# Optimization experiments

Measured on AMD Instinct MI355X. Metric: run time of the kernel, lower is better.

The kernel has to match this reference:

```python
import jax, jax.numpy as jnp
import numpy as np

B, S, H, E, V, EXTRA = 128, 512, 1024, 1024, 50000, 500
EPS = 1e-8


def setup_inputs() -> dict:
    key = jax.random.key(0)
    ks = jax.random.split(key, 32)
    sc = 0.02
    n = lambda k, sh: (jax.random.normal(k, sh, jnp.float32) * sc)
    return {
        'inputs': jax.random.randint(ks[0], (B, 1), 0, V),
        'dec_hidden': n(ks[1], (1, B, H)),
        'enc_outputs': n(ks[2], (B, S, H)),
        'enc_padding_mask': jnp.zeros((B, S), jnp.float32),
        'context_vector_t1': n(ks[3], (B, H)),
        'enc_batch_extend_vocab': jax.random.randint(ks[4], (B, S), 0, V + EXTRA),
        'extra_zeros': jnp.zeros((B, EXTRA), jnp.float32),
        'coverage': jax.random.uniform(ks[5], (B, S), jnp.float32) * 0.1,
        # parameters
        'embed': n(ks[6], (V, E)),
        'ln_g': jnp.ones((E,), jnp.float32),
        'ln_b': jnp.zeros((E,), jnp.float32),
        'xc_W': n(ks[7], (E, H + E)), 'xc_b': jnp.zeros((E,), jnp.float32),
        'W_ih': n(ks[8], (3 * H, E)), 'W_hh': n(ks[9], (3 * H, H)),
        'b_ih': jnp.zeros((3 * H,), jnp.float32), 'b_hh': jnp.zeros((3 * H,), jnp.float32),
        'Wh': n(ks[10], (H, H)),
        'Ws': n(ks[11], (H, H)), 'Ws_b': jnp.zeros((H,), jnp.float32),
        'Wc': n(ks[12], (H, 1)),
        'Vv': n(ks[13], (H,)),
        'pg_W': n(ks[14], (2 * H + E,)), 'pg_b': jnp.zeros((1,), jnp.float32),
        'out1_W': n(ks[15], (H, 2 * H)), 'out1_b': jnp.zeros((H,), jnp.float32),
        'out2_W': n(ks[16], (V, H)), 'out2_b': jnp.zeros((V,), jnp.float32),
    }


def _layernorm(x, g, b):
    mu = jnp.mean(x, axis=-1, keepdims=True)
    var = jnp.mean(jnp.square(x - mu), axis=-1, keepdims=True)
    return (x - mu) / jnp.sqrt(var + 1e-5) * g + b


def reference(inputs, dec_hidden, enc_outputs, enc_padding_mask, context_vector_t1,
              enc_batch_extend_vocab, extra_zeros, coverage,
              embed, ln_g, ln_b, xc_W, xc_b, W_ih, W_hh, b_ih, b_hh,
              Wh, Ws, Ws_b, Wc, Vv, pg_W, pg_b, out1_W, out1_b, out2_W, out2_b):
    # embedding + layernorm: [B, E]
    x = _layernorm(embed[inputs[:, 0]], ln_g, ln_b)
    # x_context: Linear(H+E -> E)
    x = jnp.concatenate([x, context_vector_t1], axis=1) @ xc_W.T + xc_b

    # single GRU step (torch gate order r, z, n)
    h0 = dec_hidden[0]  # [B, H]
    gx = x @ W_ih.T + b_ih
    gh = h0 @ W_hh.T + b_hh
    r = jax.nn.sigmoid(gx[:, :H] + gh[:, :H])
    z = jax.nn.sigmoid(gx[:, H:2 * H] + gh[:, H:2 * H])
    nn_ = jnp.tanh(gx[:, 2 * H:] + r * gh[:, 2 * H:])
    s_t = (1.0 - z) * nn_ + z * h0  # [B, H]; dec_output == s_t for 1-layer GRU
    dec_output = s_t

    # Bahdanau additive attention with coverage
    enc_feat = jnp.einsum('bsh,kh->bsk', enc_outputs, Wh)           # [B,S,H]
    dec_feat = s_t @ Ws.T + Ws_b                                     # [B,H]
    cov_feat = coverage[:, :, None] * Wc[:, 0][None, None, :]        # [B,S,H]
    e_t = jnp.einsum('bsh,h->bs', jnp.tanh(enc_feat + dec_feat[:, None, :] + cov_feat), Vv)
    atten_dist = jax.nn.softmax(e_t + enc_padding_mask, axis=1)      # [B,S]
    h_t = jnp.einsum('bs,bsh->bh', atten_dist, enc_outputs)          # [B,H]
    coverage_next = coverage + atten_dist

    # pointer generator gate
    p_gen_in = jnp.concatenate([h_t, s_t, x], axis=1)                # [B, 2H+E]
    p_gen = jnp.clip(jax.nn.sigmoid(p_gen_in @ pg_W + pg_b), EPS, None)[:, None]  # [B,1]

    # vocab distribution
    s_t_h_t = jnp.concatenate([dec_output, h_t], axis=1)             # [B,2H]
    logits = (s_t_h_t @ out1_W.T + out1_b) @ out2_W.T + out2_b       # [B,V]
    vocab_dist = jax.nn.softmax(logits, axis=1)

    # mix + scatter-add copy distribution over extended vocab
    vocab_dist_ = jnp.concatenate([p_gen * vocab_dist, extra_zeros], axis=1)  # [B, V+EXTRA]
    atten_dist_ = (1.0 - p_gen) * atten_dist
    rows = jnp.arange(B)[:, None]
    final_dist = vocab_dist_.at[rows, enc_batch_extend_vocab].add(atten_dist_)
    final_dist = jnp.clip(final_dist, EPS, None)

    coverage_loss = jnp.sum(jnp.minimum(atten_dist, coverage_next), axis=1)  # [B]
    return (jnp.log(final_dist), s_t[None], h_t, coverage_next, coverage_loss)
```

## Files before the change

### kernel.cpp

```cpp
#include <hip/hip_runtime.h>
#include <hip/hip_bf16.h>
#include <stdint.h>

#define B_ 128
#define S_ 512
#define H_ 1024
#define E_ 1024
#define V_ 50000
#define EXTRA_ 500
#define VE_ 50500
#define EPS_ 1e-8f

typedef __attribute__((ext_vector_type(4))) float f32x4;
typedef __attribute__((ext_vector_type(8))) short bf16x8;

__device__ __forceinline__ unsigned short f2bf(float f) {
    unsigned u = __builtin_bit_cast(unsigned, f);
    u = (u + 0x7FFFu + ((u >> 16) & 1u)) >> 16;
    return (unsigned short)u;
}

__device__ __forceinline__ bf16x8 pack8(const float* f) {
    union { bf16x8 v; unsigned short s[8]; } u;
#pragma unroll
    for (int i = 0; i < 8; ++i) u.s[i] = f2bf(f[i]);
    return u.v;
}

__device__ __forceinline__ float bf2f(unsigned short s) {
    unsigned u = (unsigned)s << 16;
    return __builtin_bit_cast(float, u);
}

__device__ __forceinline__ float fast_tanh(float x) {
    x = fminf(fmaxf(x, -15.f), 15.f);
    float e = __expf(2.f * x);
    return __fdividef(e - 1.f, e + 1.f);
}

__device__ __forceinline__ void gload16(const void* g, void* l) {
    __builtin_amdgcn_global_load_lds(
        reinterpret_cast<const __attribute__((address_space(1))) unsigned int*>(
            reinterpret_cast<uintptr_t>(g)),
        reinterpret_cast<__attribute__((address_space(3))) unsigned int*>(
            reinterpret_cast<uintptr_t>(l)),
        16, 0, 0);
}

__global__ __launch_bounds__(256) void prep_kernel(
    const float* __restrict__ enc, const float* __restrict__ wh,
    unsigned short* __restrict__ enc_bf, unsigned short* __restrict__ wh_bf,
    const int* __restrict__ tok, const float* __restrict__ embed,
    const float* __restrict__ g, const float* __restrict__ beta,
    const float* __restrict__ ctx, float* __restrict__ x_cat)
{
    __shared__ float red[256];
    int bid = blockIdx.x, t = threadIdx.x;
    if (bid < 33280) {
        const float* in; unsigned short* out; int i;
        if (bid < 512) { in = wh;  out = wh_bf;  i = (bid * 256 + t) * 8; }
        else           { in = enc; out = enc_bf; i = ((bid - 512) * 256 + t) * 8; }
        float f[8];
        *(float4*)f     = *(const float4*)(in + i);
        *(float4*)(f+4) = *(const float4*)(in + i + 4);
        union { uint4 v; unsigned short s[8]; } u;
#pragma unroll
        for (int j = 0; j < 8; ++j) u.s[j] = f2bf(f[j]);
        *(uint4*)(out + i) = u.v;
        return;
    }
    int b = bid - 33280;
    const float* row = embed + (size_t)tok[b] * E_;
    float v[4];
    float s = 0.f;
#pragma unroll
    for (int i = 0; i < 4; ++i) { v[i] = row[t + i*256]; s += v[i]; }
    red[t] = s; __syncthreads();
    for (int o = 128; o > 0; o >>= 1) { if (t < o) red[t] += red[t+o]; __syncthreads(); }
    float mu = red[0] * (1.f/E_);
    __syncthreads();
    s = 0.f;
#pragma unroll
    for (int i = 0; i < 4; ++i) { float d = v[i]-mu; s += d*d; }
    red[t] = s; __syncthreads();
    for (int o = 128; o > 0; o >>= 1) { if (t < o) red[t] += red[t+o]; __syncthreads(); }
    float inv = rsqrtf(red[0]*(1.f/E_) + 1e-5f);
    float* xrow = x_cat + (size_t)b * 2048;
#pragma unroll
    for (int i = 0; i < 4; ++i) {
        int j = t + i*256;
        xrow[j] = (v[i]-mu)*inv*g[j] + beta[j];
        xrow[1024 + j] = ctx[b*1024 + j];
    }
}

__global__ __launch_bounds__(256) void embed_ln_kernel(
    const int* __restrict__ tok, const float* __restrict__ embed,
    const float* __restrict__ g, const float* __restrict__ beta,
    const float* __restrict__ ctx, float* __restrict__ x_cat)
{
    __shared__ float red[256];
    int b = blockIdx.x, t = threadIdx.x;
    const float* row = embed + (size_t)tok[b] * E_;
    float v[4];
    float s = 0.f;
#pragma unroll
    for (int i = 0; i < 4; ++i) { v[i] = row[t + i*256]; s += v[i]; }
    red[t] = s; __syncthreads();
    for (int o = 128; o > 0; o >>= 1) { if (t < o) red[t] += red[t+o]; __syncthreads(); }
    float mu = red[0] * (1.f/E_);
    __syncthreads();
    s = 0.f;
#pragma unroll
    for (int i = 0; i < 4; ++i) { float d = v[i]-mu; s += d*d; }
    red[t] = s; __syncthreads();
    for (int o = 128; o > 0; o >>= 1) { if (t < o) red[t] += red[t+o]; __syncthreads(); }
    float inv = rsqrtf(red[0]*(1.f/E_) + 1e-5f);
    float* xrow = x_cat + (size_t)b * 2048;
#pragma unroll
    for (int i = 0; i < 4; ++i) {
        int j = t + i*256;
        xrow[j] = (v[i]-mu)*inv*g[j] + beta[j];
        xrow[1024 + j] = ctx[b*1024 + j];
    }
}

__global__ __launch_bounds__(256) void gemm128_kernel(
    const float* __restrict__ A, const float* __restrict__ W,
    const float* __restrict__ bias, float* __restrict__ C,
    int N, int K, int ldc, int kchunk)
{
    __shared__ char Ab[128*64*2];
    __shared__ char Wb[64*64*2];
    const int t = threadIdx.x;
    const int wid = t >> 6, lane = t & 63;
    const int waveM = wid >> 1, waveN = wid & 1;
    const int lq = lane >> 4, lr = lane & 15;
    const int n0 = blockIdx.x * 64;
    const int kbeg = blockIdx.y * kchunk, kend = kbeg + kchunk;
    f32x4 acc[4][2];
#pragma unroll
    for (int i = 0; i < 4; ++i)
#pragma unroll
        for (int j = 0; j < 2; ++j) acc[i][j] = (f32x4){0.f,0.f,0.f,0.f};
    for (int kc = kbeg; kc < kend; kc += 64) {
        __syncthreads();
#pragma unroll
        for (int i = 0; i < 4; ++i) {
            int c = t + i*256;
            int row = c >> 3, k8 = (c & 7) << 3;
            const float* src = A + (size_t)row*K + kc + k8;
            float f[8];
            *(float4*)f     = *(const float4*)src;
            *(float4*)(f+4) = *(const float4*)(src+4);
            int byte = row*128 + ((k8*2) ^ ((row&7)<<4));
            *(bf16x8*)(Ab + byte) = pack8(f);
        }
#pragma unroll
        for (int i = 0; i < 2; ++i) {
            int c = t + i*256;
            int row = c >> 3, k8 = (c & 7) << 3;
            int n = n0 + row;
            float f[8] = {0,0,0,0,0,0,0,0};
            if (n < N) {
                const float* src = W + (size_t)n*K + kc + k8;
                *(float4*)f     = *(const float4*)src;
                *(float4*)(f+4) = *(const float4*)(src+4);
            }
            int byte = row*128 + ((k8*2) ^ ((row&7)<<4));
            *(bf16x8*)(Wb + byte) = pack8(f);
        }
        __syncthreads();
#pragma unroll
        for (int kf = 0; kf < 2; ++kf) {
            int kk2 = (kf*32 + (lq<<3)) * 2;
            bf16x8 bfr[2];
#pragma unroll
            for (int nf = 0; nf < 2; ++nf) {
                int r = waveN*32 + nf*16 + lr;
                bfr[nf] = *(const bf16x8*)(Wb + r*128 + (kk2 ^ ((r&7)<<4)));
            }
#pragma unroll
            for (int mf = 0; mf < 4; ++mf) {
                int r = waveM*64 + mf*16 + lr;
                bf16x8 afr = *(const bf16x8*)(Ab + r*128 + (kk2 ^ ((r&7)<<4)));
#pragma unroll
                for (int nf = 0; nf < 2; ++nf)
                    acc[mf][nf] = __builtin_amdgcn_mfma_f32_16x16x32_bf16(afr, bfr[nf], acc[mf][nf], 0, 0, 0);
            }
        }
    }
    float* Cp = C + (size_t)blockIdx.y * 128 * (size_t)ldc;
    bool addb = (bias != nullptr) && (blockIdx.y == 0);
#pragma unroll
    for (int mf = 0; mf < 4; ++mf)
#pragma unroll
        for (int nf = 0; nf < 2; ++nf) {
            int n = n0 + waveN*32 + nf*16 + lr;
            if (n < N) {
                float bv = addb ? bias[n] : 0.f;
#pragma unroll
                for (int r = 0; r < 4; ++r) {
                    int m = waveM*64 + mf*16 + (lq<<2) + r;
                    Cp[(size_t)m*ldc + n] = acc[mf][nf][r] + bv;
                }
            }
        }
}

__global__ __launch_bounds__(256) void gemm128_dual_kernel(
    const float* __restrict__ A0, const float* __restrict__ W0,
    const float* __restrict__ b0, float* __restrict__ C0, int ap0,
    const float* __restrict__ A1, const float* __restrict__ W1,
    const float* __restrict__ b1, float* __restrict__ C1, int ap1,
    int N, int K, int ldc, int kchunk)
{
    __shared__ char Ab[128*64*2];
    __shared__ char Wb[64*64*2];
    const float* A = blockIdx.z ? A1 : A0;
    const float* W = blockIdx.z ? W1 : W0;
    const float* bias = blockIdx.z ? b1 : b0;
    float* C = blockIdx.z ? C1 : C0;
    const int ap = blockIdx.z ? ap1 : ap0;
    const int t = threadIdx.x;
    const int wid = t >> 6, lane = t & 63;
    const int waveM = wid >> 1, waveN = wid & 1;
    const int lq = lane >> 4, lr = lane & 15;
    const int n0 = blockIdx.x * 64;
    const int kbeg = blockIdx.y * kchunk, kend = kbeg + kchunk;
    f32x4 acc[4][2];
#pragma unroll
    for (int i = 0; i < 4; ++i)
#pragma unroll
        for (int j = 0; j < 2; ++j) acc[i][j] = (f32x4){0.f,0.f,0.f,0.f};
    for (int kc = kbeg; kc < kend; kc += 64) {
        __syncthreads();
#pragma unroll
        for (int i = 0; i < 4; ++i) {
            int c = t + i*256;
            int row = c >> 3, k8 = (c & 7) << 3;
            const float* src = A + (size_t)row*K + kc + k8;
            float f[8];
            *(float4*)f     = *(const float4*)src;
            *(float4*)(f+4) = *(const float4*)(src+4);
            if (ap == 4) {
#pragma unroll
                for (int p = 1; p < 4; ++p) {
                    float g0[8];
                    *(float4*)g0     = *(const float4*)(src + p*131072);
                    *(float4*)(g0+4) = *(const float4*)(src + p*131072 + 4);
#pragma unroll
                    for (int j = 0; j < 8; ++j) f[j] += g0[j];
                }
            }
            int byte = row*128 + ((k8*2) ^ ((row&7)<<4));
            *(bf16x8*)(Ab + byte) = pack8(f);
        }
#pragma unroll
        for (int i = 0; i < 2; ++i) {
            int c = t + i*256;
            int row = c >> 3, k8 = (c & 7) << 3;
            int n = n0 + row;
            float f[8] = {0,0,0,0,0,0,0,0};
            if (n < N) {
                const float* src = W + (size_t)n*K + kc + k8;
                *(float4*)f     = *(const float4*)src;
                *(float4*)(f+4) = *(const float4*)(src+4);
            }
            int byte = row*128 + ((k8*2) ^ ((row&7)<<4));
            *(bf16x8*)(Wb + byte) = pack8(f);
        }
        __syncthreads();
#pragma unroll
        for (int kf = 0; kf < 2; ++kf) {
            int kk2 = (kf*32 + (lq<<3)) * 2;
            bf16x8 bfr[2];
#pragma unroll
            for (int nf = 0; nf < 2; ++nf) {
                int r = waveN*32 + nf*16 + lr;
                bfr[nf] = *(const bf16x8*)(Wb + r*128 + (kk2 ^ ((r&7)<<4)));
            }
#pragma unroll
            for (int mf = 0; mf < 4; ++mf) {
                int r = waveM*64 + mf*16 + lr;
                bf16x8 afr = *(const bf16x8*)(Ab + r*128 + (kk2 ^ ((r&7)<<4)));
#pragma unroll
                for (int nf = 0; nf < 2; ++nf)
                    acc[mf][nf] = __builtin_amdgcn_mfma_f32_16x16x32_bf16(afr, bfr[nf], acc[mf][nf], 0, 0, 0);
            }
        }
    }
    float* Cp = C + (size_t)blockIdx.y * 128 * (size_t)ldc;
    bool addb = (bias != nullptr) && (blockIdx.y == 0);
#pragma unroll
    for (int mf = 0; mf < 4; ++mf)
#pragma unroll
        for (int nf = 0; nf < 2; ++nf) {
            int n = n0 + waveN*32 + nf*16 + lr;
            if (n < N) {
                float bv = addb ? bias[n] : 0.f;
#pragma unroll
                for (int r = 0; r < 4; ++r) {
                    int m = waveM*64 + mf*16 + (lq<<2) + r;
                    Cp[(size_t)m*ldc + n] = acc[mf][nf][r] + bv;
                }
            }
        }
}

__global__ __launch_bounds__(256) void reduce4_kernel(
    const float* __restrict__ in, float* __restrict__ out, int len)
{
    int i = blockIdx.x*256 + threadIdx.x;
    if (i < len) out[i] = in[i] + in[len+i] + in[2*len+i] + in[3*len+i];
}

__global__ __launch_bounds__(256) void gru_gate_kernel(
    const float* __restrict__ gxp, const float* __restrict__ ghp,
    const float* __restrict__ h0, float* __restrict__ s_t)
{
    int i = blockIdx.x*256 + threadIdx.x;
    int b = i >> 10, h = i & 1023;
    const float* gx0 = gxp + (size_t)b*3072;
    const float* gx1 = gx0 + 393216;
    const float* gh0 = ghp + (size_t)b*3072;
    const float* gh1 = gh0 + 393216;
    float grx = gx0[h] + gx1[h],        grh = gh0[h] + gh1[h];
    float gzx = gx0[h+1024]+gx1[h+1024], gzh = gh0[h+1024]+gh1[h+1024];
    float gnx = gx0[h+2048]+gx1[h+2048], gnh = gh0[h+2048]+gh1[h+2048];
    float r = 1.f/(1.f+__expf(-(grx + grh)));
    float z = 1.f/(1.f+__expf(-(gzx + gzh)));
    float n = fast_tanh(gnx + r*gnh);
    s_t[i] = (1.f-z)*n + z*h0[i];
}

__global__ __launch_bounds__(256,4) void attn_gemm_bf16_kernel(
    const unsigned short* __restrict__ encb,
    const unsigned short* __restrict__ whb,
    const float* __restrict__ ds_part,
    const float* __restrict__ coverage,
    const float* __restrict__ Wc, const float* __restrict__ Vv,
    float* __restrict__ e_part)
{
    __shared__ char Ab[128*128];
    __shared__ char Bb[128*128];
    const int t = threadIdx.x;
    const int wid = t >> 6, lane = t & 63;
    const int waveM = wid >> 1, waveN = wid & 1;
    const int lq = lane >> 4, lr = lane & 15;
    int bid = blockIdx.x;
    int wg = (bid & 7) * 512 + (bid >> 3);
    const int nt = wg & 7, mt = wg >> 3;
    const int m0 = mt * 128, n0 = nt * 128;
    const int b = m0 >> 9;

    const int grow = wid*8 + (lane >> 3);
    const int gk16 = (lane & 7) ^ ((lane >> 3) & 7);
    const unsigned short* asrc = encb + (size_t)(m0 + grow)*H_ + gk16*8;
    const unsigned short* bsrc = whb  + (size_t)(n0 + grow)*H_ + gk16*8;
    char* aldst = Ab + wid*1024;
    char* bldst = Bb + wid*1024;

    f32x4 acc[4][4];
#pragma unroll
    for (int i = 0; i < 4; ++i)
#pragma unroll
        for (int j = 0; j < 4; ++j) acc[i][j] = (f32x4){0.f,0.f,0.f,0.f};

    for (int kc = 0; kc < 1024; kc += 64) {
        __syncthreads();
#pragma unroll
        for (int i = 0; i < 4; ++i) {
            gload16(asrc + kc + i*32*H_, aldst + i*4096);
            gload16(bsrc + kc + i*32*H_, bldst + i*4096);
        }
        __syncthreads();
#pragma unroll
        for (int kf = 0; kf < 2; ++kf) {
            const int koff = kf*64 + lq*16;
            bf16x8 bfr[4];
#pragma unroll
            for (int nf = 0; nf < 4; ++nf) {
                int r = waveN*64 + nf*16 + lr;
                bfr[nf] = *(const bf16x8*)(Bb + r*128 + (koff ^ ((r&7)<<4)));
            }
#pragma unroll
            for (int mf = 0; mf < 4; ++mf) {
                int r = waveM*64 + mf*16 + lr;
                bf16x8 afr = *(const bf16x8*)(Ab + r*128 + (koff ^ ((r&7)<<4)));
#pragma unroll
                for (int nf = 0; nf < 4; ++nf)
                    acc[mf][nf] = __builtin_amdgcn_mfma_f32_16x16x32_bf16(afr, bfr[nf], acc[mf][nf], 0, 0, 0);
            }
        }
    }
    float cv[4][4];
#pragma unroll
    for (int mf = 0; mf < 4; ++mf)
#pragma unroll
        for (int r = 0; r < 4; ++r) {
            int m = m0 + waveM*64 + mf*16 + lq*4 + r;
            cv[mf][r] = coverage[b*S_ + (m & 511)];
        }
    float e_acc[4][4] = {};
#pragma unroll
    for (int nf = 0; nf < 4; ++nf) {
        int n = n0 + waveN*64 + nf*16 + lr;
        const float* dsp = ds_part + b*H_ + n;
        float df = dsp[0] + dsp[131072] + dsp[262144] + dsp[393216];
        float wc = Wc[n];
        float vv = Vv[n];
#pragma unroll
        for (int mf = 0; mf < 4; ++mf)
#pragma unroll
            for (int r = 0; r < 4; ++r)
                e_acc[mf][r] += fast_tanh(acc[mf][nf][r] + df + cv[mf][r]*wc) * vv;
    }
#pragma unroll
    for (int msk = 1; msk < 16; msk <<= 1)
#pragma unroll
        for (int mf = 0; mf < 4; ++mf)
#pragma unroll
            for (int r = 0; r < 4; ++r)
                e_acc[mf][r] += __shfl_xor(e_acc[mf][r], msk);
    __syncthreads();
    float* el = (float*)Ab;
    if (lr == 0) {
#pragma unroll
        for (int mf = 0; mf < 4; ++mf)
#pragma unroll
            for (int r = 0; r < 4; ++r)
                el[waveN*128 + waveM*64 + mf*16 + lq*4 + r] = e_acc[mf][r];
    }
    __syncthreads();
    if (t < 128)
        e_part[(size_t)nt*65536 + m0 + t] = el[t] + el[128 + t];
}

__global__ __launch_bounds__(512,4) void attn_gemm_f32_kernel(
    const float* __restrict__ enc, const float* __restrict__ Wh,
    const float* __restrict__ ds_part, const float* __restrict__ coverage,
    const float* __restrict__ Wc, const float* __restrict__ Vv,
    float* __restrict__ e_part)
{
    __shared__ char Ab[128*64*2];
    __shared__ char Bb[256*64*2];
    __shared__ float e_lds[4][128];
    const int t = threadIdx.x;
    const int wid = t >> 6, lane = t & 63;
    const int waveM = wid >> 2, waveN = wid & 3;
    const int lq = lane >> 4, lr = lane & 15;
    int bid = blockIdx.x;
    int wg = (bid & 7) * 256 + (bid >> 3);
    const int mt = wg >> 2, nt = wg & 3;
    const int m0 = mt * 128, n0 = nt * 256;
    const int b = m0 >> 9;
    const int arow = t >> 2, ak0 = (t & 3) * 16;
    const int brow = t >> 1, bk0 = (t & 1) * 32;
    f32x4 acc[4][4];
#pragma unroll
    for (int i = 0; i < 4; ++i)
#pragma unroll
        for (int j = 0; j < 4; ++j) acc[i][j] = (f32x4){0.f,0.f,0.f,0.f};
    for (int kc = 0; kc < 1024; kc += 64) {
        __syncthreads();
        {
            const float* src = enc + (size_t)(m0 + arow)*H_ + kc + ak0;
            float f[16];
            *(float4*)(f)    = *(const float4*)(src);
            *(float4*)(f+4)  = *(const float4*)(src+4);
            *(float4*)(f+8)  = *(const float4*)(src+8);
            *(float4*)(f+12) = *(const float4*)(src+12);
            char* dst = Ab + arow*128;
            int sw = (arow & 7) << 4;
            *(bf16x8*)(dst + ((ak0*2)      ^ sw)) = pack8(f);
            *(bf16x8*)(dst + ((ak0*2 + 16) ^ sw)) = pack8(f+8);
        }
        {
            const float* src = Wh + (size_t)(n0 + brow)*H_ + kc + bk0;
            char* dst = Bb + brow*128;
            int sw = (brow & 7) << 4;
            float f[16];
            *(float4*)(f)    = *(const float4*)(src);
            *(float4*)(f+4)  = *(const float4*)(src+4);
            *(float4*)(f+8)  = *(const float4*)(src+8);
            *(float4*)(f+12) = *(const float4*)(src+12);
            *(bf16x8*)(dst + ((bk0*2)      ^ sw)) = pack8(f);
            *(bf16x8*)(dst + ((bk0*2 + 16) ^ sw)) = pack8(f+8);
            *(float4*)(f)    = *(const float4*)(src+16);
            *(float4*)(f+4)  = *(const float4*)(src+20);
            *(float4*)(f+8)  = *(const float4*)(src+24);
            *(float4*)(f+12) = *(const float4*)(src+28);
            *(bf16x8*)(dst + ((bk0*2 + 32) ^ sw)) = pack8(f);
            *(bf16x8*)(dst + ((bk0*2 + 48) ^ sw)) = pack8(f+8);
        }
        __syncthreads();
#pragma unroll
        for (int kf = 0; kf < 2; ++kf) {
            const int koff = kf*64 + lq*16;
            bf16x8 bfr[4];
#pragma unroll
            for (int nf = 0; nf < 4; ++nf) {
                int r = waveN*64 + nf*16 + lr;
                bfr[nf] = *(const bf16x8*)(Bb + r*128 + (koff ^ ((r&7)<<4)));
            }
#pragma unroll
            for (int mf = 0; mf < 4; ++mf) {
                int r = waveM*64 + mf*16 + lr;
                bf16x8 afr = *(const bf16x8*)(Ab + r*128 + (koff ^ ((r&7)<<4)));
#pragma unroll
                for (int nf = 0; nf < 4; ++nf)
                    acc[mf][nf] = __builtin_amdgcn_mfma_f32_16x16x32_bf16(afr, bfr[nf], acc[mf][nf], 0, 0, 0);
            }
        }
    }
    float cv[4][4];
#pragma unroll
    for (int mf = 0; mf < 4; ++mf)
#pragma unroll
        for (int r = 0; r < 4; ++r) {
            int m = m0 + waveM*64 + mf*16 + lq*4 + r;
            cv[mf][r] = coverage[b*S_ + (m & 511)];
        }
    float e_acc[4][4] = {};
#pragma unroll
    for (int nf = 0; nf < 4; ++nf) {
        int n = n0 + waveN*64 + nf*16 + lr;
        const float* dsp = ds_part + b*H_ + n;
        float df = dsp[0] + dsp[131072] + dsp[262144] + dsp[393216];
        float wc = Wc[n];
        float vv = Vv[n];
#pragma unroll
        for (int mf = 0; mf < 4; ++mf)
#pragma unroll
            for (int r = 0; r < 4; ++r)
                e_acc[mf][r] += fast_tanh(acc[mf][nf][r] + df + cv[mf][r]*wc) * vv;
    }
#pragma unroll
    for (int msk = 1; msk < 16; msk <<= 1)
#pragma unroll
        for (int mf = 0; mf < 4; ++mf)
#pragma unroll
            for (int r = 0; r < 4; ++r)
                e_acc[mf][r] += __shfl_xor(e_acc[mf][r], msk);
    if (lr == 0) {
#pragma unroll
        for (int mf = 0; mf < 4; ++mf)
#pragma unroll
            for (int r = 0; r < 4; ++r)
                e_lds[waveN][waveM*64 + mf*16 + lq*4 + r] = e_acc[mf][r];
    }
    __syncthreads();
    if (t < 128)
        e_part[(size_t)nt*65536 + m0 + t] = e_lds[0][t] + e_lds[1][t] + e_lds[2][t] + e_lds[3][t];
}

__global__ __launch_bounds__(256) void attn_softmax_kernel(
    const float* __restrict__ e_part, int np, const float* __restrict__ mask,
    const float* __restrict__ cov, float* __restrict__ att,
    float* __restrict__ cov_next, float* __restrict__ loss)
{
    __shared__ float red[256];
    int b = blockIdx.x, t = threadIdx.x;
    int i1 = b*S_ + t, i2 = i1 + 256;
    float e1 = mask[i1], e2 = mask[i2];
    for (int p = 0; p < np; ++p) { e1 += e_part[(size_t)p*65536 + i1]; e2 += e_part[(size_t)p*65536 + i2]; }
    red[t] = fmaxf(e1, e2); __syncthreads();
    for (int o = 128; o > 0; o >>= 1) { if (t < o) red[t] = fmaxf(red[t], red[t+o]); __syncthreads(); }
    float m = red[0]; __syncthreads();
    float a1 = __expf(e1-m), a2 = __expf(e2-m);
    red[t] = a1+a2; __syncthreads();
    for (int o = 128; o > 0; o >>= 1) { if (t < o) red[t] += red[t+o]; __syncthreads(); }
    float inv = 1.f/red[0]; __syncthreads();
    a1 *= inv; a2 *= inv;
    att[i1] = a1; att[i2] = a2;
    float c1 = cov[i1]+a1, c2 = cov[i2]+a2;
    cov_next[i1] = c1; cov_next[i2] = c2;
    red[t] = fminf(a1,c1)+fminf(a2,c2); __syncthreads();
    for (int o = 128; o > 0; o >>= 1) { if (t < o) red[t] += red[t+o]; __syncthreads(); }
    if (t == 0) loss[b] = red[0];
}

__global__ __launch_bounds__(256) void smax_ctx_bf16_kernel(
    const float* __restrict__ e_part, const float* __restrict__ mask,
    const float* __restrict__ cov, const unsigned short* __restrict__ encb,
    float* __restrict__ att, float* __restrict__ cov_next, float* __restrict__ loss,
    float* __restrict__ hq)
{
    __shared__ float red[256];
    __shared__ float asl[512];
    __shared__ float cpart[128][9];
    int b = blockIdx.x, q = blockIdx.y, t = threadIdx.x;
    int i1 = b*S_ + t, i2 = i1 + 256;
    float e1 = mask[i1], e2 = mask[i2];
#pragma unroll
    for (int p = 0; p < 8; ++p) { e1 += e_part[(size_t)p*65536 + i1]; e2 += e_part[(size_t)p*65536 + i2]; }
    red[t] = fmaxf(e1, e2); __syncthreads();
    for (int o = 128; o > 0; o >>= 1) { if (t < o) red[t] = fmaxf(red[t], red[t+o]); __syncthreads(); }
    float m = red[0]; __syncthreads();
    float a1 = __expf(e1-m), a2 = __expf(e2-m);
    red[t] = a1+a2; __syncthreads();
    for (int o = 128; o > 0; o >>= 1) { if (t < o) red[t] += red[t+o]; __syncthreads(); }
    float inv = 1.f/red[0]; __syncthreads();
    a1 *= inv; a2 *= inv;
    asl[t] = a1; asl[t+256] = a2;
    if (q == 0) {
        att[i1] = a1; att[i2] = a2;
        float c1 = cov[i1]+a1, c2 = cov[i2]+a2;
        cov_next[i1] = c1; cov_next[i2] = c2;
        red[t] = fminf(a1,c1)+fminf(a2,c2); __syncthreads();
        for (int o = 128; o > 0; o >>= 1) { if (t < o) red[t] += red[t+o]; __syncthreads(); }
        if (t == 0) loss[b] = red[0];
    }
    __syncthreads();
    int lane = t & 127, su = t >> 7;
    int hc = lane * 8;
    const unsigned short* ep = encb + ((size_t)(b*S_ + q*128 + su*64))*H_ + hc;
    const float* aw = asl + q*128 + su*64;
    float acc[8] = {};
#pragma unroll 2
    for (int s = 0; s < 64; ++s) {
        uint4 v = *(const uint4*)(ep + (size_t)s*H_);
        float w = aw[s];
        const unsigned short* pv = (const unsigned short*)&v;
#pragma unroll
        for (int k = 0; k < 8; ++k) acc[k] += w * bf2f(pv[k]);
    }
    if (su == 1) {
#pragma unroll
        for (int k = 0; k < 8; ++k) cpart[lane][k] = acc[k];
    }
    __syncthreads();
    if (su == 0) {
        float o[8];
#pragma unroll
        for (int k = 0; k < 8; ++k) o[k] = acc[k] + cpart[lane][k];
        float* dst = hq + (size_t)q*131072 + (size_t)b*1024 + hc;
        *(float4*)dst     = *(float4*)o;
        *(float4*)(dst+4) = *(float4*)(o+4);
    }
}

__global__ __launch_bounds__(256) void context_part_f32_kernel(
    const float* __restrict__ att, const float* __restrict__ enc, float* __restrict__ hq)
{
    __shared__ float asl[128];
    int b = blockIdx.x, sub = blockIdx.y;
    int hh = sub & 1, q = sub >> 1;
    int t = threadIdx.x;
    if (t < 128) asl[t] = att[b*S_ + q*128 + t];
    __syncthreads();
    int h = hh*512 + t*2;
    const float* ep = enc + (size_t)b*S_*H_ + (size_t)q*128*H_ + h;
    float a0 = 0.f, a1 = 0.f;
#pragma unroll 4
    for (int s = 0; s < 128; ++s) {
        float2 v = *(const float2*)(ep + (size_t)s*H_);
        float w = asl[s];
        a0 += w*v.x; a1 += w*v.y;
    }
    float* o = hq + ((size_t)q*B_ + b)*H_ + h;
    o[0] = a0; o[1] = a1;
}

__global__ __launch_bounds__(256) void pgen_kernel(
    const float* __restrict__ hq, const float* __restrict__ s_t, const float* __restrict__ x_part,
    const float* __restrict__ pgW, const float* __restrict__ pgb,
    float* __restrict__ pgen, float* __restrict__ h_t, float* __restrict__ A2)
{
    __shared__ float red[256];
    int b = blockIdx.x, t = threadIdx.x;
    float dot = 0.f;
#pragma unroll
    for (int i = 0; i < 4; ++i) {
        int j = t + i*256;
        const float* hp = hq + (size_t)b*1024 + j;
        float hv = hp[0] + hp[131072] + hp[262144] + hp[393216];
        const float* xp = x_part + (size_t)b*1024 + j;
        float xv = xp[0] + xp[131072] + xp[262144] + xp[393216];
        float sv = s_t[b*1024 + j];
        h_t[b*1024 + j] = hv;
        A2[(size_t)b*2048 + j] = sv;
        A2[(size_t)b*2048 + 1024 + j] = hv;
        dot += hv*pgW[j] + sv*pgW[1024+j] + xv*pgW[2048+j];
    }
    red[t] = dot; __syncthreads();
    for (int o = 128; o > 0; o >>= 1) { if (t < o) red[t] += red[t+o]; __syncthreads(); }
    if (t == 0) {
        float p = 1.f/(1.f+__expf(-(red[0] + pgb[0])));
        pgen[b] = fmaxf(p, EPS_);
    }
}

__global__ __launch_bounds__(256) void vocab_pass1_kernel(
    const float* __restrict__ logits, float2* __restrict__ mpart)
{
    __shared__ float rm[256], rl[256];
    int b = blockIdx.x, c = blockIdx.y, t = threadIdx.x;
    int lo = c * 12625;
    int hi = min(lo + 12625, V_);
    const float* row = logits + (size_t)b*VE_;
    float m = -1e30f, l = 0.f;
    for (int i = lo + t; i < hi; i += 256) {
        float v = row[i];
        if (v > m) { l = l*__expf(m-v) + 1.f; m = v; }
        else l += __expf(v-m);
    }
    rm[t] = m; rl[t] = l; __syncthreads();
    for (int o = 128; o > 0; o >>= 1) {
        if (t < o) {
            float m1 = rm[t], m2 = rm[t+o];
            float M = fmaxf(m1, m2);
            rl[t] = rl[t]*__expf(m1-M) + rl[t+o]*__expf(m2-M);
            rm[t] = M;
        }
        __syncthreads();
    }
    if (t == 0) mpart[b*4 + c] = make_float2(rm[0], rl[0]);
}

__global__ __launch_bounds__(256) void vocab_pass2_kernel(
    const float* __restrict__ logits, const float2* __restrict__ mpart,
    const float* __restrict__ pgen, const int* __restrict__ ebev,
    const float* __restrict__ att, float* __restrict__ out0)
{
    __shared__ unsigned bmap[395];
    __shared__ unsigned hkey[1024];
    __shared__ float hval[1024];
    int b = blockIdx.x, c = blockIdx.y, t = threadIdx.x;
    int lo = c * 12625, hi = lo + 12625;
    float2 q0 = mpart[b*4+0], q1 = mpart[b*4+1], q2 = mpart[b*4+2], q3 = mpart[b*4+3];
    float M = fmaxf(fmaxf(q0.x, q1.x), fmaxf(q2.x, q3.x));
    float L = q0.y*__expf(q0.x-M) + q1.y*__expf(q1.x-M) + q2.y*__expf(q2.x-M) + q3.y*__expf(q3.x-M);
    float pg = pgen[b];
    float inv = pg / L;
    for (int i = t; i < 395; i += 256) bmap[i] = 0u;
    for (int i = t; i < 1024; i += 256) { hkey[i] = 0xFFFFFFFFu; hval[i] = 0.f; }
    __syncthreads();
    for (int s = t; s < 512; s += 256) {
        int col = ebev[b*S_ + s];
        if (col >= lo && col < hi) {
            float v = (1.f - pg) * att[b*S_ + s];
            unsigned cl = (unsigned)(col - lo);
            atomicOr(&bmap[cl >> 5], 1u << (cl & 31));
            unsigned slot = (cl * 2654435761u >> 16) & 1023u;
            while (true) {
                unsigned old = atomicCAS(&hkey[slot], 0xFFFFFFFFu, cl);
                if (old == 0xFFFFFFFFu || old == cl) { atomicAdd(&hval[slot], v); break; }
                slot = (slot + 1) & 1023u;
            }
        }
    }
    __syncthreads();
    const float* row = logits + (size_t)b*VE_;
    float* orow = out0 + (size_t)b*VE_;
    for (int i = lo + t; i < hi; i += 256) {
        float base = 0.f;
        if (i < V_) base = __expf(row[i] - M) * inv;
        unsigned cl = (unsigned)(i - lo);
        if (bmap[cl >> 5] & (1u << (cl & 31))) {
            unsigned slot = (cl * 2654435761u >> 16) & 1023u;
            while (hkey[slot] != cl) slot = (slot + 1) & 1023u;
            base += hval[slot];
        }
        orow[i] = __logf(fmaxf(base, EPS_));
    }
}

extern "C" void kernel_launch(void* const* d_in, const int* in_sizes, int n_in,
                              void* d_out, int out_size, void* d_ws, size_t ws_size,
                              hipStream_t stream) {
    const int*   tok        = (const int*)d_in[0];
    const float* dec_hidden = (const float*)d_in[1];
    const float* enc        = (const float*)d_in[2];
    const float* mask       = (const float*)d_in[3];
    const float* ctx1       = (const float*)d_in[4];
    const int*   ebev       = (const int*)d_in[5];
    const float* cov        = (const float*)d_in[7];
    const float* embed      = (const float*)d_in[8];
    const float* ln_g       = (const float*)d_in[9];
    const float* ln_b       = (const float*)d_in[10];
    const float* xc_W       = (const float*)d_in[11];
    const float* xc_b       = (const float*)d_in[12];
    const float* W_ih       = (const float*)d_in[13];
    const float* W_hh       = (const float*)d_in[14];
    const float* b_ih       = (const float*)d_in[15];
    const float* b_hh       = (const float*)d_in[16];
    const float* Wh         = (const float*)d_in[17];
    const float* Ws         = (const float*)d_in[18];
    const float* Ws_b       = (const float*)d_in[19];
    const float* Wc         = (const float*)d_in[20];
    const float* Vv         = (const float*)d_in[21];
    const float* pg_W       = (const float*)d_in[22];
    const float* pg_b       = (const float*)d_in[23];
    const float* out1_W     = (const float*)d_in[24];
    const float* out1_b     = (const float*)d_in[25];
    const float* out2_W     = (const float*)d_in[26];
    const float* out2_b     = (const float*)d_in[27];

    float* out      = (float*)d_out;
    float* s_t      = out + 6464000;
    float* h_t      = out + 6595072;
    float* cov_next = out + 6726144;
    float* loss     = out + 6791680;

    const size_t ENC_SLOTS = 33554432, WH_SLOTS = 524288;
    const size_t BASE_SLOTS = 5178496;
    const size_t need = (ENC_SLOTS + WH_SLOTS + BASE_SLOTS) * 4;
    const bool bf16_path = (ws_size >= need);

    float* wsf = (float*)d_ws;
    unsigned short* enc_bf = (unsigned short*)d_ws;
    unsigned short* wh_bf  = (unsigned short*)(wsf + ENC_SLOTS);
    float* base     = bf16_path ? (wsf + ENC_SLOTS + WH_SLOTS) : wsf;
    float* x_cat    = base;
    float* x_part   = base + 262144;
    float* x        = base + 786432;
    float* gx_part  = base + 917504;
    float* gh_part  = base + 1703936;
    float* ds_part  = base + 2490368;
    float* e_part   = base + 3145728;
    float* att      = base + 3670016;
    float* pgen     = base + 3735552;
    float* A2       = base + 3735680;
    float* h2_part  = base + 3997824;
    float* h2       = base + 4522112;
    float* hq       = base + 4653184;
    float2* mpart   = (float2*)(base + 5177472);

    if (bf16_path) {
        prep_kernel<<<33408, 256, 0, stream>>>(enc, Wh, enc_bf, wh_bf,
                                               tok, embed, ln_g, ln_b, ctx1, x_cat);
    } else {
        embed_ln_kernel<<<128, 256, 0, stream>>>(tok, embed, ln_g, ln_b, ctx1, x_cat);
    }
    gemm128_kernel<<<dim3(16,4), 256, 0, stream>>>(x_cat, xc_W, xc_b, x_part, 1024, 2048, 1024, 512);
    gemm128_dual_kernel<<<dim3(48,2,2), 256, 0, stream>>>(
        x_part, W_ih, b_ih, gx_part, 4,
        dec_hidden, W_hh, b_hh, gh_part, 1, 3072, 1024, 3072, 512);
    gru_gate_kernel<<<512, 256, 0, stream>>>(gx_part, gh_part, dec_hidden, s_t);
    gemm128_kernel<<<dim3(16,4), 256, 0, stream>>>(s_t, Ws, Ws_b, ds_part, 1024, 1024, 1024, 256);

    if (bf16_path) {
        attn_gemm_bf16_kernel<<<4096, 256, 0, stream>>>(enc_bf, wh_bf, ds_part, cov, Wc, Vv, e_part);
        dim3 g8(128, 4);
        smax_ctx_bf16_kernel<<<g8, 256, 0, stream>>>(e_part, mask, cov, enc_bf,
                                                     att, cov_next, loss, hq);
    } else {
        attn_gemm_f32_kernel<<<2048, 512, 0, stream>>>(enc, Wh, ds_part, cov, Wc, Vv, e_part);
        attn_softmax_kernel<<<128, 256, 0, stream>>>(e_part, 4, mask, cov, att, cov_next, loss);
        dim3 g8(128, 8);
        context_part_f32_kernel<<<g8, 256, 0, stream>>>(att, enc, hq);
    }
    pgen_kernel<<<128, 256, 0, stream>>>(hq, s_t, x_part, pg_W, pg_b, pgen, h_t, A2);
    gemm128_kernel<<<dim3(16,4), 256, 0, stream>>>(A2, out1_W, out1_b, h2_part, 1024, 2048, 1024, 512);
    reduce4_kernel<<<512, 256, 0, stream>>>(h2_part, h2, 131072);

    gemm128_kernel<<<dim3(782,1), 256, 0, stream>>>(h2, out2_W, out2_b, out, 50000, 1024, VE_, 1024);
    vocab_pass1_kernel<<<dim3(128,4), 256, 0, stream>>>(out, mpart);
    vocab_pass2_kernel<<<dim3(128,4), 256, 0, stream>>>(out, mpart, pgen, ebev, att, out);
}
```

Measured before the change: 496.4 us.

## Fuse vocab softmax partials into output GEMM epilogue and GRU gates into Ws GEMM

The vocab projection GEMM now computes per-block online-softmax (max, sum) partials in its epilogue. This removes the separate pass1 kernel that re-read the 128x50000 logits, and pass2 combines 782 partials per row instead of 4. The GRU gate computation is folded into the A-tile load of the Ws GEMM, removing the gru_gate kernel launch and the s_t round trip. The cost is that every column block recomputes the gate math redundantly, and the GEMM epilogue gains extra shuffles and syncs.

```diff
diff --git a/kernel.cpp b/kernel.cpp
--- a/kernel.cpp
+++ b/kernel.cpp
@@ -10,6 +10,7 @@
 #define EXTRA_ 500
 #define VE_ 50500
 #define EPS_ 1e-8f
+#define NLB_ 782
 
 typedef __attribute__((ext_vector_type(4))) float f32x4;
 typedef __attribute__((ext_vector_type(8))) short bf16x8;
@@ -36,6 +37,11 @@
     x = fminf(fmaxf(x, -15.f), 15.f);
     float e = __expf(2.f * x);
     return __fdividef(e - 1.f, e + 1.f);
+}
+
+__device__ __forceinline__ void ld8(float* d, const float* p) {
+    *(float4*)d     = *(const float4*)p;
+    *(float4*)(d+4) = *(const float4*)(p+4);
 }
 
 __device__ __forceinline__ void gload16(const void* g, void* l) {
@@ -61,8 +67,7 @@
         if (bid < 512) { in = wh;  out = wh_bf;  i = (bid * 256 + t) * 8; }
         else           { in = enc; out = enc_bf; i = ((bid - 512) * 256 + t) * 8; }
         float f[8];
-        *(float4*)f     = *(const float4*)(in + i);
-        *(float4*)(f+4) = *(const float4*)(in + i + 4);
+        ld8(f, in + i);
         union { uint4 v; unsigned short s[8]; } u;
 #pragma unroll
         for (int j = 0; j < 8; ++j) u.s[j] = f2bf(f[j]);
@@ -128,7 +133,7 @@
 __global__ __launch_bounds__(256) void gemm128_kernel(
     const float* __restrict__ A, const float* __restrict__ W,
     const float* __restrict__ bias, float* __restrict__ C,
-    int N, int K, int ldc, int kchunk)
+    int N, int K, int ldc, int kchunk, float2* __restrict__ lpart)
 {
     __shared__ char Ab[128*64*2];
     __shared__ char Wb[64*64*2];
@@ -151,8 +156,7 @@
             int row = c >> 3, k8 = (c & 7) << 3;
             const float* src = A + (size_t)row*K + kc + k8;
             float f[8];
-            *(float4*)f     = *(const float4*)src;
-            *(float4*)(f+4) = *(const float4*)(src+4);
+            ld8(f, src);
             int byte = row*128 + ((k8*2) ^ ((row&7)<<4));
             *(bf16x8*)(Ab + byte) = pack8(f);
         }
@@ -162,11 +166,7 @@
             int row = c >> 3, k8 = (c & 7) << 3;
             int n = n0 + row;
             float f[8] = {0,0,0,0,0,0,0,0};
-            if (n < N) {
-                const float* src = W + (size_t)n*K + kc + k8;
-                *(float4*)f     = *(const float4*)src;
-                *(float4*)(f+4) = *(const float4*)(src+4);
-            }
+            if (n < N) ld8(f, W + (size_t)n*K + kc + k8);
             int byte = row*128 + ((k8*2) ^ ((row&7)<<4));
             *(bf16x8*)(Wb + byte) = pack8(f);
         }
@@ -206,6 +206,43 @@
                 }
             }
         }
+    if (lpart != nullptr) {
+        __syncthreads();
+        float2* pp = (float2*)Ab;
+#pragma unroll
+        for (int mf = 0; mf < 4; ++mf)
+#pragma unroll
+            for (int r = 0; r < 4; ++r) {
+                float m = -1e30f, s = 0.f;
+#pragma unroll
+                for (int nf = 0; nf < 2; ++nf) {
+                    int n = n0 + waveN*32 + nf*16 + lr;
+                    if (n < N) {
+                        float v = acc[mf][nf][r] + bias[n];
+                        float M2 = fmaxf(m, v);
+                        s = s*__expf(m - M2) + __expf(v - M2);
+                        m = M2;
+                    }
+                }
+#pragma unroll
+                for (int msk = 1; msk < 16; msk <<= 1) {
+                    float om = __shfl_xor(m, msk);
+                    float os = __shfl_xor(s, msk);
+                    float M2 = fmaxf(m, om);
+                    s = s*__expf(m - M2) + os*__expf(om - M2);
+                    m = M2;
+                }
+                if (lr == 0)
+                    pp[waveN*128 + waveM*64 + mf*16 + (lq<<2) + r] = make_float2(m, s);
+            }
+        __syncthreads();
+        if (t < 128) {
+            float2 a = pp[t], b2 = pp[128 + t];
+            float M2 = fmaxf(a.x, b2.x);
+            float S = a.y*__expf(a.x - M2) + b2.y*__expf(b2.x - M2);
+            lpart[(size_t)t*NLB_ + blockIdx.x] = make_float2(M2, S);
+        }
+    }
 }
 
 __global__ __launch_bounds__(256) void gemm128_dual_kernel(
@@ -241,14 +278,12 @@
             int row = c >> 3, k8 = (c & 7) << 3;
             const float* src = A + (size_t)row*K + kc + k8;
             float f[8];
-            *(float4*)f     = *(const float4*)src;
-            *(float4*)(f+4) = *(const float4*)(src+4);
+            ld8(f, src);
             if (ap == 4) {
 #pragma unroll
                 for (int p = 1; p < 4; ++p) {
                     float g0[8];
-                    *(float4*)g0     = *(const float4*)(src + p*131072);
-                    *(float4*)(g0+4) = *(const float4*)(src + p*131072 + 4);
+                    ld8(g0, src + p*131072);
 #pragma unroll
                     for (int j = 0; j < 8; ++j) f[j] += g0[j];
                 }
@@ -262,11 +297,7 @@
             int row = c >> 3, k8 = (c & 7) << 3;
             int n = n0 + row;
             float f[8] = {0,0,0,0,0,0,0,0};
-            if (n < N) {
-                const float* src = W + (size_t)n*K + kc + k8;
-                *(float4*)f     = *(const float4*)src;
-                *(float4*)(f+4) = *(const float4*)(src+4);
-            }
+            if (n < N) ld8(f, W + (size_t)n*K + kc + k8);
             int byte = row*128 + ((k8*2) ^ ((row&7)<<4));
             *(bf16x8*)(Wb + byte) = pack8(f);
         }
@@ -308,30 +339,121 @@
         }
 }
 
+__global__ __launch_bounds__(256) void gemm_gru_kernel(
+    const float* __restrict__ gxp, const float* __restrict__ ghp,
+    const float* __restrict__ h0, float* __restrict__ s_t,
+    const float* __restrict__ W, const float* __restrict__ bias,
+    float* __restrict__ C, int kchunk)
+{
+    __shared__ char Ab[128*64*2];
+    __shared__ char Wb[64*64*2];
+    const int t = threadIdx.x;
+    const int wid = t >> 6, lane = t & 63;
+    const int waveM = wid >> 1, waveN = wid & 1;
+    const int lq = lane >> 4, lr = lane & 15;
+    const int n0 = blockIdx.x * 64;
+    const int kbeg = blockIdx.y * kchunk, kend = kbeg + kchunk;
+    f32x4 acc[4][2];
+#pragma unroll
+    for (int i = 0; i < 4; ++i)
+#pragma unroll
+        for (int j = 0; j < 2; ++j) acc[i][j] = (f32x4){0.f,0.f,0.f,0.f};
+    for (int kc = kbeg; kc < kend; kc += 64) {
+        __syncthreads();
+#pragma unroll
+        for (int i = 0; i < 4; ++i) {
+            int c = t + i*256;
+            int row = c >> 3, k8 = (c & 7) << 3;
+            int k = kc + k8;
+            const float* gx0 = gxp + (size_t)row*3072 + k;
+            const float* gx1 = gx0 + 393216;
+            const float* gh0 = ghp + (size_t)row*3072 + k;
+            const float* gh1 = gh0 + 393216;
+            float a0[8], a1[8], rr[8], rh[8], zz[8], zh[8], nn[8], nh[8], hv[8], f[8];
+            ld8(a0, gx0);        ld8(a1, gx1);
+#pragma unroll
+            for (int j = 0; j < 8; ++j) rr[j] = a0[j] + a1[j];
+            ld8(a0, gh0);        ld8(a1, gh1);
+#pragma unroll
+            for (int j = 0; j < 8; ++j) rh[j] = a0[j] + a1[j];
+            ld8(a0, gx0+1024);   ld8(a1, gx1+1024);
+#pragma unroll
+            for (int j = 0; j < 8; ++j) zz[j] = a0[j] + a1[j];
+            ld8(a0, gh0+1024);   ld8(a1, gh1+1024);
+#pragma unroll
+            for (int j = 0; j < 8; ++j) zh[j] = a0[j] + a1[j];
+            ld8(a0, gx0+2048);   ld8(a1, gx1+2048);
+#pragma unroll
+            for (int j = 0; j < 8; ++j) nn[j] = a0[j] + a1[j];
+            ld8(a0, gh0+2048);   ld8(a1, gh1+2048);
+#pragma unroll
+            for (int j = 0; j < 8; ++j) nh[j] = a0[j] + a1[j];
+            ld8(hv, h0 + (size_t)row*1024 + k);
+#pragma unroll
+            for (int j = 0; j < 8; ++j) {
+                float r = 1.f/(1.f+__expf(-(rr[j] + rh[j])));
+                float z = 1.f/(1.f+__expf(-(zz[j] + zh[j])));
+                float n = fast_tanh(nn[j] + r*nh[j]);
+                f[j] = (1.f-z)*n + z*hv[j];
+            }
+            if (blockIdx.x == 0) {
+                float* dst = s_t + (size_t)row*1024 + k;
+                *(float4*)dst     = *(float4*)f;
+                *(float4*)(dst+4) = *(float4*)(f+4);
+            }
+            int byte = row*128 + ((k8*2) ^ ((row&7)<<4));
+            *(bf16x8*)(Ab + byte) = pack8(f);
+        }
+#pragma unroll
+        for (int i = 0; i < 2; ++i) {
+            int c = t + i*256;
+            int row = c >> 3, k8 = (c & 7) << 3;
+            float f[8];
+            ld8(f, W + (size_t)(n0 + row)*1024 + kc + k8);
+            int byte = row*128 + ((k8*2) ^ ((row&7)<<4));
+            *(bf16x8*)(Wb + byte) = pack8(f);
+        }
+        __syncthreads();
+#pragma unroll
+        for (int kf = 0; kf < 2; ++kf) {
+            int kk2 = (kf*32 + (lq<<3)) * 2;
+            bf16x8 bfr[2];
+#pragma unroll
+            for (int nf = 0; nf < 2; ++nf) {
+                int r = waveN*32 + nf*16 + lr;
+                bfr[nf] = *(const bf16x8*)(Wb + r*128 + (kk2 ^ ((r&7)<<4)));
+            }
+#pragma unroll
+            for (int mf = 0; mf < 4; ++mf) {
+                int r = waveM*64 + mf*16 + lr;
+                bf16x8 afr = *(const bf16x8*)(Ab + r*128 + (kk2 ^ ((r&7)<<4)));
+#pragma unroll
+                for (int nf = 0; nf < 2; ++nf)
+                    acc[mf][nf] = __builtin_amdgcn_mfma_f32_16x16x32_bf16(afr, bfr[nf], acc[mf][nf], 0, 0, 0);
+            }
+        }
+    }
+    float* Cp = C + (size_t)blockIdx.y * 128 * 1024;
+    bool addb = (blockIdx.y == 0);
+#pragma unroll
+    for (int mf = 0; mf < 4; ++mf)
+#pragma unroll
+        for (int nf = 0; nf < 2; ++nf) {
+            int n = n0 + waveN*32 + nf*16 + lr;
+            float bv = addb ? bias[n] : 0.f;
+#pragma unroll
+            for (int r = 0; r < 4; ++r) {
+                int m = waveM*64 + mf*16 + (lq<<2) + r;
+                Cp[(size_t)m*1024 + n] = acc[mf][nf][r] + bv;
+            }
+        }
+}
+
 __global__ __launch_bounds__(256) void reduce4_kernel(
     const float* __restrict__ in, float* __restrict__ out, int len)
 {
     int i = blockIdx.x*256 + threadIdx.x;
     if (i < len) out[i] = in[i] + in[len+i] + in[2*len+i] + in[3*len+i];
-}
-
-__global__ __launch_bounds__(256) void gru_gate_kernel(
-    const float* __restrict__ gxp, const float* __restrict__ ghp,
-    const float* __restrict__ h0, float* __restrict__ s_t)
-{
-    int i = blockIdx.x*256 + threadIdx.x;
-    int b = i >> 10, h = i & 1023;
-    const float* gx0 = gxp + (size_t)b*3072;
-    const float* gx1 = gx0 + 393216;
-    const float* gh0 = ghp + (size_t)b*3072;
-    const float* gh1 = gh0 + 393216;
-    float grx = gx0[h] + gx1[h],        grh = gh0[h] + gh1[h];
-    float gzx = gx0[h+1024]+gx1[h+1024], gzh = gh0[h+1024]+gh1[h+1024];
-    float gnx = gx0[h+2048]+gx1[h+2048], gnh = gh0[h+2048]+gh1[h+2048];
-    float r = 1.f/(1.f+__expf(-(grx + grh)));
-    float z = 1.f/(1.f+__expf(-(gzx + gzh)));
-    float n = fast_tanh(gnx + r*gnh);
-    s_t[i] = (1.f-z)*n + z*h0[i];
 }
 
 __global__ __launch_bounds__(256,4) void attn_gemm_bf16_kernel(
@@ -467,10 +589,7 @@
         {
             const float* src = enc + (size_t)(m0 + arow)*H_ + kc + ak0;
             float f[16];
-            *(float4*)(f)    = *(const float4*)(src);
-            *(float4*)(f+4)  = *(const float4*)(src+4);
-            *(float4*)(f+8)  = *(const float4*)(src+8);
-            *(float4*)(f+12) = *(const float4*)(src+12);
+            ld8(f, src); ld8(f+8, src+8);
             char* dst = Ab + arow*128;
             int sw = (arow & 7) << 4;
             *(bf16x8*)(dst + ((ak0*2)      ^ sw)) = pack8(f);
@@ -481,16 +600,10 @@
             char* dst = Bb + brow*128;
             int sw = (brow & 7) << 4;
             float f[16];
-            *(float4*)(f)    = *(const float4*)(src);
-            *(float4*)(f+4)  = *(const float4*)(src+4);
-            *(float4*)(f+8)  = *(const float4*)(src+8);
-            *(float4*)(f+12) = *(const float4*)(src+12);
+            ld8(f, src); ld8(f+8, src+8);
             *(bf16x8*)(dst + ((bk0*2)      ^ sw)) = pack8(f);
             *(bf16x8*)(dst + ((bk0*2 + 16) ^ sw)) = pack8(f+8);
-            *(float4*)(f)    = *(const float4*)(src+16);
-            *(float4*)(f+4)  = *(const float4*)(src+20);
-            *(float4*)(f+8)  = *(const float4*)(src+24);
-            *(float4*)(f+12) = *(const float4*)(src+28);
+            ld8(f, src+16); ld8(f+8, src+24);
             *(bf16x8*)(dst + ((bk0*2 + 32) ^ sw)) = pack8(f);
             *(bf16x8*)(dst + ((bk0*2 + 48) ^ sw)) = pack8(f+8);
         }
@@ -692,55 +805,45 @@
     }
 }
 
-__global__ __launch_bounds__(256) void vocab_pass1_kernel(
-    const float* __restrict__ logits, float2* __restrict__ mpart)
-{
-    __shared__ float rm[256], rl[256];
-    int b = blockIdx.x, c = blockIdx.y, t = threadIdx.x;
-    int lo = c * 12625;
-    int hi = min(lo + 12625, V_);
-    const float* row = logits + (size_t)b*VE_;
-    float m = -1e30f, l = 0.f;
-    for (int i = lo + t; i < hi; i += 256) {
-        float v = row[i];
-        if (v > m) { l = l*__expf(m-v) + 1.f; m = v; }
-        else l += __expf(v-m);
-    }
-    rm[t] = m; rl[t] = l; __syncthreads();
-    for (int o = 128; o > 0; o >>= 1) {
-        if (t < o) {
-            float m1 = rm[t], m2 = rm[t+o];
-            float M = fmaxf(m1, m2);
-            rl[t] = rl[t]*__expf(m1-M) + rl[t+o]*__expf(m2-M);
-            rm[t] = M;
-        }
-        __syncthreads();
-    }
-    if (t == 0) mpart[b*4 + c] = make_float2(rm[0], rl[0]);
-}
-
 __global__ __launch_bounds__(256) void vocab_pass2_kernel(
-    const float* __restrict__ logits, const float2* __restrict__ mpart,
+    const float* __restrict__ logits, const float2* __restrict__ lpart,
     const float* __restrict__ pgen, const int* __restrict__ ebev,
     const float* __restrict__ att, float* __restrict__ out0)
 {
     __shared__ unsigned bmap[395];
     __shared__ unsigned hkey[1024];
     __shared__ float hval[1024];
+    __shared__ float rm[256], rl[256];
     int b = blockIdx.x, c = blockIdx.y, t = threadIdx.x;
     int lo = c * 12625, hi = lo + 12625;
-    float2 q0 = mpart[b*4+0], q1 = mpart[b*4+1], q2 = mpart[b*4+2], q3 = mpart[b*4+3];
-    float M = fmaxf(fmaxf(q0.x, q1.x), fmaxf(q2.x, q3.x));
-    float L = q0.y*__expf(q0.x-M) + q1.y*__expf(q1.x-M) + q2.y*__expf(q2.x-M) + q3.y*__expf(q3.x-M);
+    for (int i = t; i < 395; i += 256) bmap[i] = 0u;
+    for (int i = t; i < 1024; i += 256) { hkey[i] = 0xFFFFFFFFu; hval[i] = 0.f; }
+    float m = -1e30f, s = 0.f;
+    for (int i = t; i < NLB_; i += 256) {
+        float2 p = lpart[(size_t)b*NLB_ + i];
+        float M2 = fmaxf(m, p.x);
+        s = s*__expf(m - M2) + p.y*__expf(p.x - M2);
+        m = M2;
+    }
+    rm[t] = m; rl[t] = s;
+    __syncthreads();
+    for (int o = 128; o > 0; o >>= 1) {
+        if (t < o) {
+            float m1 = rm[t], s1 = rl[t];
+            float m2 = rm[t+o], s2 = rl[t+o];
+            float M2 = fmaxf(m1, m2);
+            rl[t] = s1*__expf(m1-M2) + s2*__expf(m2-M2);
+            rm[t] = M2;
+        }
+        __syncthreads();
+    }
+    float M = rm[0], L = rl[0];
     float pg = pgen[b];
     float inv = pg / L;
-    for (int i = t; i < 395; i += 256) bmap[i] = 0u;
-    for (int i = t; i < 1024; i += 256) { hkey[i] = 0xFFFFFFFFu; hval[i] = 0.f; }
-    __syncthreads();
-    for (int s = t; s < 512; s += 256) {
-        int col = ebev[b*S_ + s];
+    for (int sx = t; sx < 512; sx += 256) {
+        int col = ebev[b*S_ + sx];
         if (col >= lo && col < hi) {
-            float v = (1.f - pg) * att[b*S_ + s];
+            float v = (1.f - pg) * att[b*S_ + sx];
             unsigned cl = (unsigned)(col - lo);
             atomicOr(&bmap[cl >> 5], 1u << (cl & 31));
             unsigned slot = (cl * 2654435761u >> 16) & 1023u;
@@ -805,7 +908,7 @@
     float* loss     = out + 6791680;
 
     const size_t ENC_SLOTS = 33554432, WH_SLOTS = 524288;
-    const size_t BASE_SLOTS = 5178496;
+    const size_t BASE_SLOTS = 5177472 + 200192;
     const size_t need = (ENC_SLOTS + WH_SLOTS + BASE_SLOTS) * 4;
     const bool bf16_path = (ws_size >= need);
 
@@ -815,7 +918,6 @@
     float* base     = bf16_path ? (wsf + ENC_SLOTS + WH_SLOTS) : wsf;
     float* x_cat    = base;
     float* x_part   = base + 262144;
-    float* x        = base + 786432;
     float* gx_part  = base + 917504;
     float* gh_part  = base + 1703936;
     float* ds_part  = base + 2490368;
@@ -826,7 +928,7 @@
     float* h2_part  = base + 3997824;
     float* h2       = base + 4522112;
     float* hq       = base + 4653184;
-    float2* mpart   = (float2*)(base + 5177472);
+    float2* lpart   = (float2*)(base + 5177472);
 
     if (bf16_path) {
         prep_kernel<<<33408, 256, 0, stream>>>(enc, Wh, enc_bf, wh_bf,
@@ -834,12 +936,12 @@
     } else {
         embed_ln_kernel<<<128, 256, 0, stream>>>(tok, embed, ln_g, ln_b, ctx1, x_cat);
     }
-    gemm128_kernel<<<dim3(16,4), 256, 0, stream>>>(x_cat, xc_W, xc_b, x_part, 1024, 2048, 1024, 512);
+    gemm128_kernel<<<dim3(16,4), 256, 0, stream>>>(x_cat, xc_W, xc_b, x_part, 1024, 2048, 1024, 512, nullptr);
     gemm128_dual_kernel<<<dim3(48,2,2), 256, 0, stream>>>(
         x_part, W_ih, b_ih, gx_part, 4,
         dec_hidden, W_hh, b_hh, gh_part, 1, 3072, 1024, 3072, 512);
-    gru_gate_kernel<<<512, 256, 0, stream>>>(gx_part, gh_part, dec_hidden, s_t);
-    gemm128_kernel<<<dim3(16,4), 256, 0, stream>>>(s_t, Ws, Ws_b, ds_part, 1024, 1024, 1024, 256);
+    gemm_gru_kernel<<<dim3(16,4), 256, 0, stream>>>(gx_part, gh_part, dec_hidden, s_t,
+                                                    Ws, Ws_b, ds_part, 256);
 
     if (bf16_path) {
         attn_gemm_bf16_kernel<<<4096, 256, 0, stream>>>(enc_bf, wh_bf, ds_part, cov, Wc, Vv, e_part);
@@ -853,10 +955,9 @@
         context_part_f32_kernel<<<g8, 256, 0, stream>>>(att, enc, hq);
     }
     pgen_kernel<<<128, 256, 0, stream>>>(hq, s_t, x_part, pg_W, pg_b, pgen, h_t, A2);
-    gemm128_kernel<<<dim3(16,4), 256, 0, stream>>>(A2, out1_W, out1_b, h2_part, 1024, 2048, 1024, 512);
+    gemm128_kernel<<<dim3(16,4), 256, 0, stream>>>(A2, out1_W, out1_b, h2_part, 1024, 2048, 1024, 512, nullptr);
     reduce4_kernel<<<512, 256, 0, stream>>>(h2_part, h2, 131072);
 
-    gemm128_kernel<<<dim3(782,1), 256, 0, stream>>>(h2, out2_W, out2_b, out, 50000, 1024, VE_, 1024);
-    vocab_pass1_kernel<<<dim3(128,4), 256, 0, stream>>>(out, mpart);
-    vocab_pass2_kernel<<<dim3(128,4), 256, 0, stream>>>(out, mpart, pgen, ebev, att, out);
-}
+    gemm128_kernel<<<dim3(NLB_,1), 256, 0, stream>>>(h2, out2_W, out2_b, out, 50000, 1024, VE_, 1024, lpart);
+    vocab_pass2_kernel<<<dim3(128,4), 256, 0, stream>>>(out, lpart, pgen, ebev, att, out);
+}
```

New measurement: 514.0 us. 1.04x slower.
